# Performance work log

Measured on AMD Instinct MI355X. Metric: run time of the kernel, lower is better.

Reference implementation:

```python
import jax, jax.numpy as jnp
import numpy as np

V, D, B, L = 100000, 64, 4096, 200

def setup_inputs() -> dict:
    key = jax.random.key(0)
    ks = jax.random.split(key, 10)
    s = 0.05  # keep activations in a sane range for sigmoid
    return {
        "item_ids": jax.random.randint(ks[0], (B,), 0, V),
        "history": jax.random.randint(ks[1], (B, L), 0, V),
        "hist_len": jax.random.randint(ks[2], (B,), 1, L + 1),
        "emb_table": jax.random.normal(ks[3], (V, D), jnp.float32) * s,
        "aW1": jax.random.normal(ks[4], (3 * D, D), jnp.float32) * s,
        "ab1": jnp.zeros((D,), jnp.float32),
        "aW2": jax.random.normal(ks[5], (D, 1), jnp.float32) * s,
        "ab2": jnp.zeros((1,), jnp.float32),
        "fW1": jax.random.normal(ks[6], (3 * D, 128), jnp.float32) * s,
        "fb1": jnp.zeros((128,), jnp.float32),
        "fW2": jax.random.normal(ks[7], (128, 64), jnp.float32) * s,
        "fb2": jnp.zeros((64,), jnp.float32),
        "fW3": jax.random.normal(ks[8], (64, 1), jnp.float32) * s,
        "fb3": jnp.zeros((1,), jnp.float32),
    }

def reference(item_ids, history, hist_len, emb_table, aW1, ab1, aW2, ab2,
              fW1, fb1, fW2, fb2, fW3, fb3):
    target = emb_table[item_ids]                      # [B, D]
    hist = emb_table[history]                         # [B, L, D]
    # original pads short histories with zero rows -> zero the padded tail
    mask = (jnp.arange(hist.shape[1])[None, :] < hist_len[:, None]).astype(hist.dtype)
    hist = hist * mask[..., None]
    tgt = jnp.broadcast_to(target[:, None, :], hist.shape)     # [B, L, D]
    # attention_fc takes 3*D features: (hist, target, hist*target)
    feat = jnp.concatenate([hist, tgt, hist * tgt], axis=-1)   # [B, L, 3D]
    h = jax.nn.relu(feat @ aW1 + ab1)                 # [B, L, D]
    scores = (h @ aW2 + ab2)[..., 0]                  # [B, L]
    # faithful to original: softmax over full padded length (no length mask)
    w = jax.nn.softmax(scores, axis=1)
    pooled = jnp.einsum('bl,bld->bd', w, hist)        # [B, D]
    comb = jnp.concatenate([target, pooled, pooled - target], axis=-1)  # [B, 3D]
    z = jax.nn.relu(comb @ fW1 + fb1)
    z = jax.nn.relu(z @ fW2 + fb2)
    return jax.nn.sigmoid(z @ fW3 + fb3)              # [B, 1]
```

## Files before the change

kernel.cpp:

```cpp
#include <hip/hip_runtime.h>
#include <hip/hip_bf16.h>

#define NV 100000
#define ND 64
#define NB 4096
#define NL 200
#define MT 13

typedef __bf16 bf16_t;
typedef __bf16 bf16x8 __attribute__((ext_vector_type(8)));
typedef __bf16 bf16x4 __attribute__((ext_vector_type(4)));
typedef float f32x4 __attribute__((ext_vector_type(4)));

#define TB_ELEMS ((long)NV * ND)
#define TBV (TB_ELEMS / 8)
#define FT1 (128 * 192)
#define FT2 (64 * 128)
#define ZPV 64
#define CVT_TASKS (TBV + FT1 + FT2 + ZPV)

__global__ __launch_bounds__(256)
void cvt_kernel(const float* __restrict__ emb,
                const float* __restrict__ fW1,
                const float* __restrict__ fW2,
                bf16_t* __restrict__ tb,
                bf16_t* __restrict__ fW1T,
                bf16_t* __restrict__ fW2T,
                bf16_t* __restrict__ zpage)
{
    long t = (long)blockIdx.x * 256 + threadIdx.x;
    if (t >= CVT_TASKS) return;
    if (t < TBV) {
        long i = t * 8;
        f32x4 a0 = *(const f32x4*)(emb + i);
        f32x4 a1 = *(const f32x4*)(emb + i + 4);
        bf16x8 o;
#pragma unroll
        for (int j = 0; j < 4; ++j) { o[j] = (bf16_t)a0[j]; o[j + 4] = (bf16_t)a1[j]; }
        *(bf16x8*)(tb + i) = o;
    } else {
        int u = (int)(t - TBV);
        if (u < FT1) {
            int n = u / 192, k = u - n * 192;
            fW1T[u] = (bf16_t)fW1[k * 128 + n];
        } else if (u < FT1 + FT2) {
            int u2 = u - FT1;
            int n = u2 >> 7, k = u2 & 127;
            fW2T[u2] = (bf16_t)fW2[k * 64 + n];
        } else {
            int u3 = u - FT1 - FT2;
            *(bf16x8*)(zpage + u3 * 8) = (bf16x8)(bf16_t)0.f;
        }
    }
}

__global__ __launch_bounds__(512, 4)
void din_kernel1(const int* __restrict__ item_ids,
                 const int* __restrict__ history,
                 const int* __restrict__ hist_len,
                 const float* __restrict__ emb,
                 const bf16_t* __restrict__ tb,
                 const bf16_t* __restrict__ zpage,
                 const float* __restrict__ aW1,
                 const float* __restrict__ ab1,
                 const float* __restrict__ aW2,
                 const bf16_t* __restrict__ fW1T, const float* __restrict__ fb1,
                 const bf16_t* __restrict__ fW2T, const float* __restrict__ fb2,
                 const float* __restrict__ fW3, const float* __restrict__ fb3,
                 float* __restrict__ out)
{
    __shared__ __align__(16) bf16_t histA[2][208 * 64];
    __shared__ __align__(16) bf16_t wbT[2][64 * 64];
    __shared__ float tgt[2][64];
    __shared__ __align__(16) float scores[2][208];
    __shared__ float wts[2][208];
    __shared__ float pp2[2][256];
    __shared__ float red[2][8];
    __shared__ float cb2[2][64];

    bf16_t* comb16 = (bf16_t*)wbT;
    bf16_t* z1s    = (bf16_t*)wbT + 3200;
    float*  z2f    = (float*)((bf16_t*)wbT + 5376);

    const int b0  = blockIdx.x * 2;
    const int tid = threadIdx.x;
    const int len0 = hist_len[b0];
    const int len1 = hist_len[b0 + 1];

    const int wave = tid >> 6, lane = tid & 63;
    const int col  = lane & 15, quad = lane >> 4;

    if (tid < 128) {
        int bx = tid >> 6, d = tid & 63;
        tgt[bx][d] = emb[(long)item_ids[b0 + bx] * ND + d];
    }

    {
        const int r = lane >> 3;
        const int c = lane & 7;
#pragma unroll
        for (int j = 0; j < 7; ++j) {
            const int R = wave * 52 + j * 8;
            const int nrows = (j == 6) ? 4 : 8;
            const int l  = R + r;
            const int bx = (l >= 208);
            const int lr = l - (bx ? 208 : 0);
            const int lenx = bx ? len1 : len0;
            const bf16_t* gsrc;
            if (lr < lenx) {
                int idx = history[(long)(b0 + bx) * NL + lr];
                gsrc = tb + (long)idx * ND + ((c ^ (lr & 7)) * 8);
            } else {
                gsrc = zpage + c * 8;
            }
            if (r < nrows) {
                __builtin_amdgcn_global_load_lds(
                    (const __attribute__((address_space(1))) void*)gsrc,
                    (__attribute__((address_space(3))) void*)(&histA[0][0] + (long)R * 64),
                    16, 0, 0);
            }
        }
    }

    {
        const int bx = wave & 1;
        const int n  = ((wave >> 1) << 4) | col;
        const int kq = quad;
        const long t0 = (long)item_ids[b0 + bx] * ND;
        f32x4 tka = *(const f32x4*)(emb + t0 + kq * 16);
        f32x4 tkb = *(const f32x4*)(emb + t0 + kq * 16 + 4);
        f32x4 tkc = *(const f32x4*)(emb + t0 + kq * 16 + 8);
        f32x4 tkd = *(const f32x4*)(emb + t0 + kq * 16 + 12);
        float csum = 0.f;
        bf16x8 w0v, w1v;
#pragma unroll
        for (int i = 0; i < 16; ++i) {
            int k = kq * 16 + i;
            float tk = (i < 4) ? tka[i] : (i < 8) ? tkb[i - 4]
                     : (i < 12) ? tkc[i - 8] : tkd[i - 12];
            float ah = aW1[k * 64 + n];
            float am = aW1[(64 + k) * 64 + n];
            float ap = aW1[(128 + k) * 64 + n];
            float wv = ah + tk * ap;
            if (i < 8) w0v[i] = (bf16_t)wv; else w1v[i - 8] = (bf16_t)wv;
            csum += tk * am;
        }
        const int S = (n & 7) << 3;
        *(bf16x8*)&wbT[bx][n * 64 + ((kq * 16    ) ^ S)] = w0v;
        *(bf16x8*)&wbT[bx][n * 64 + ((kq * 16 + 8) ^ S)] = w1v;
        csum += __shfl_xor(csum, 16, 64);
        csum += __shfl_xor(csum, 32, 64);
        if (kq == 0) cb2[bx][n] = ab1[n] + csum;
    }
    __syncthreads();

    {
        const int bx = wave & 1;
        bf16x8 afrag[4][2];
#pragma unroll
        for (int nt = 0; nt < 4; ++nt) {
            const int n = nt * 16 + col;
            const int S = (n & 7) << 3;
#pragma unroll
            for (int kb = 0; kb < 2; ++kb)
                afrag[nt][kb] = *(const bf16x8*)&wbT[bx][n * 64 + ((kb * 32 + quad * 8) ^ S)];
        }
        float cv[4][4], a2[4][4];
#pragma unroll
        for (int nt = 0; nt < 4; ++nt)
#pragma unroll
            for (int i = 0; i < 4; ++i) {
                const int no = nt * 16 + quad * 4 + i;
                cv[nt][i] = cb2[bx][no];
                a2[nt][i] = aW2[no];
            }

        for (int mt = (wave >> 1); mt < MT; mt += 4) {
            const int l = mt * 16 + col;
            const int S = (l & 7) << 3;
            const bf16_t* base = &histA[bx][l * 64];
            bf16x8 bf0 = *(const bf16x8*)&base[(     quad * 8) ^ S];
            bf16x8 bf1 = *(const bf16x8*)&base[(32 + quad * 8) ^ S];
            float sc = 0.f;
#pragma unroll
            for (int nt = 0; nt < 4; ++nt) {
                f32x4 acc = {cv[nt][0], cv[nt][1], cv[nt][2], cv[nt][3]};
                acc = __builtin_amdgcn_mfma_f32_16x16x32_bf16(afrag[nt][0], bf0, acc, 0, 0, 0);
                acc = __builtin_amdgcn_mfma_f32_16x16x32_bf16(afrag[nt][1], bf1, acc, 0, 0, 0);
#pragma unroll
                for (int i = 0; i < 4; ++i) {
                    float h = acc[i] > 0.f ? acc[i] : 0.f;
                    sc += h * a2[nt][i];
                }
            }
            sc += __shfl_xor(sc, 16, 64);
            sc += __shfl_xor(sc, 32, 64);
            if (quad == 0) scores[bx][mt * 16 + col] = sc;
        }
    }
    __syncthreads();

    {
        const int bx = tid >> 8, t = tid & 255;
        float s = (t < NL) ? scores[bx][t] : -1e30f;
        float m = s;
        for (int off = 32; off > 0; off >>= 1) m = fmaxf(m, __shfl_xor(m, off, 64));
        float e = (t < NL) ? __expf(s - m) : 0.f;
        if (t < NL) wts[bx][t] = e;
        else if (t < 208) wts[bx][t] = 0.f;
        float ss = e;
        for (int off = 32; off > 0; off >>= 1) ss += __shfl_xor(ss, off, 64);
        if ((t & 63) == 0) { red[bx][t >> 6] = m; red[bx][4 + (t >> 6)] = ss; }
    }
    __syncthreads();

    bf16x8 bw1[6]; float b1v;
    bf16x8 bw2[4]; float b2v = 0.f;
    {
        const int n = wave * 16 + col;
#pragma unroll
        for (int ks = 0; ks < 6; ++ks)
            bw1[ks] = *(const bf16x8*)&fW1T[(long)n * 192 + ks * 32 + quad * 8];
        b1v = fb1[n];
        if (wave < 4) {
            const int n2 = wave * 16 + col;
#pragma unroll
            for (int ks = 0; ks < 4; ++ks)
                bw2[ks] = *(const bf16x8*)&fW2T[(long)n2 * 128 + ks * 32 + quad * 8];
            b2v = fb2[n2];
        }
    }

    {
        const int bx = tid >> 8, t = tid & 255;
        const int c = t & 15;
        const int g = t >> 4;
        const int w4 = (tid >> 6) & 3;
        const float m0 = red[bx][0], m1 = red[bx][1], m2 = red[bx][2], m3 = red[bx][3];
        const float mg = fmaxf(fmaxf(m0, m1), fmaxf(m2, m3));
        float sc0 = __expf(m0 - mg), sc1 = __expf(m1 - mg);
        float sc2 = __expf(m2 - mg), sc3 = __expf(m3 - mg);
        const float rtot = 1.f / (sc0 * red[bx][4] + sc1 * red[bx][5] +
                                  sc2 * red[bx][6] + sc3 * red[bx][7]);
        sc0 *= rtot; sc1 *= rtot; sc2 *= rtot; sc3 *= rtot;
        f32x4 acc = {0.f, 0.f, 0.f, 0.f};
#pragma unroll
        for (int j = 0; j < 13; ++j) {
            const int l = g + j * 16;
            const float scj = (j < 4) ? sc0 : (j < 8) ? sc1 : (j < 12) ? sc2 : sc3;
            const float wl = wts[bx][l] * scj;
            bf16x4 v = *(const bf16x4*)&histA[bx][l * 64 + ((c * 4) ^ ((l & 7) << 3))];
#pragma unroll
            for (int k = 0; k < 4; ++k) acc[k] += wl * (float)v[k];
        }
#pragma unroll
        for (int k = 0; k < 4; ++k) {
            acc[k] += __shfl_xor(acc[k], 16, 64);
            acc[k] += __shfl_xor(acc[k], 32, 64);
        }
        if ((tid & 63) < 16) *(f32x4*)&pp2[bx][w4 * 64 + c * 4] = acc;
    }
    __syncthreads();

    {
        const int bx = tid >> 8, t = tid & 255;
        if (t < 192) {
            const int d = t & 63;
            float v;
            if (t < 64) v = tgt[bx][d];
            else {
                float pl = pp2[bx][d] + pp2[bx][64 + d] + pp2[bx][128 + d] + pp2[bx][192 + d];
                v = (t < 128) ? pl : pl - tgt[bx][d];
            }
            comb16[bx * 200 + t] = (bf16_t)v;
        }
    }
    __syncthreads();

    {
        f32x4 acc = {b1v, b1v, b1v, b1v};
#pragma unroll
        for (int ks = 0; ks < 6; ++ks) {
            bf16x8 a = *(const bf16x8*)&comb16[col * 200 + ks * 32 + quad * 8];
            acc = __builtin_amdgcn_mfma_f32_16x16x32_bf16(a, bw1[ks], acc, 0, 0, 0);
        }
        const int n = wave * 16 + col;
#pragma unroll
        for (int i = 0; i < 4; ++i) {
            const int m = quad * 4 + i;
            if (m < 2) z1s[m * 136 + n] = (bf16_t)fmaxf(acc[i], 0.f);
        }
    }
    __syncthreads();

    {
        if (wave < 4) {
            f32x4 acc = {b2v, b2v, b2v, b2v};
#pragma unroll
            for (int ks = 0; ks < 4; ++ks) {
                bf16x8 a = *(const bf16x8*)&z1s[col * 136 + ks * 32 + quad * 8];
                acc = __builtin_amdgcn_mfma_f32_16x16x32_bf16(a, bw2[ks], acc, 0, 0, 0);
            }
            const int n2 = wave * 16 + col;
#pragma unroll
            for (int i = 0; i < 4; ++i) {
                const int m = quad * 4 + i;
                if (m < 2) z2f[m * 64 + n2] = fmaxf(acc[i], 0.f);
            }
        }
    }
    __syncthreads();

    if (tid < 128) {
        const int bx = tid >> 6, j = tid & 63;
        float s = z2f[bx * 64 + j] * fW3[j];
        for (int off = 32; off > 0; off >>= 1) s += __shfl_xor(s, off, 64);
        if (j == 0) out[b0 + bx] = 1.f / (1.f + __expf(-(s + fb3[0])));
    }
}

extern "C" void kernel_launch(void* const* d_in, const int* in_sizes, int n_in,
                              void* d_out, int out_size, void* d_ws, size_t ws_size,
                              hipStream_t stream) {
    const int*   item_ids = (const int*)d_in[0];
    const int*   history  = (const int*)d_in[1];
    const int*   hist_len = (const int*)d_in[2];
    const float* emb      = (const float*)d_in[3];
    const float* aW1      = (const float*)d_in[4];
    const float* ab1      = (const float*)d_in[5];
    const float* aW2      = (const float*)d_in[6];
    const float* fW1      = (const float*)d_in[8];
    const float* fb1      = (const float*)d_in[9];
    const float* fW2      = (const float*)d_in[10];
    const float* fb2      = (const float*)d_in[11];
    const float* fW3      = (const float*)d_in[12];
    const float* fb3      = (const float*)d_in[13];

    bf16_t* tb    = (bf16_t*)d_ws;
    bf16_t* fW1T  = tb + TB_ELEMS;
    bf16_t* fW2T  = fW1T + FT1;
    bf16_t* zpage = fW2T + FT2;

    cvt_kernel<<<(int)((CVT_TASKS + 255) / 256), 256, 0, stream>>>(
        emb, fW1, fW2, tb, fW1T, fW2T, zpage);
    din_kernel1<<<NB / 2, 512, 0, stream>>>(item_ids, history, hist_len, emb, tb,
                                            zpage, aW1, ab1, aW2,
                                            fW1T, fb1, fW2T, fb2, fW3, fb3,
                                            (float*)d_out);
}
```

Before: 145.1 us.

## Skip padded history rows and replace async LDS gather with register staging

Replaces the global_load_lds gather (which pulled zero-page rows for padding) with per-thread register loads that fetch only valid history rows, issued before the weight-prep phase and stored to LDS after it. The attention MLP loop now runs only over 16-row tiles covering the actual history length. Padded positions get one constant score computed once from the bias term, and the pooling loop breaks early past the length. This reduces MFMA work and gather traffic for short histories, at the cost of higher register pressure from holding eight 16-byte vectors per thread across the weight-prep code.

```diff
diff --git a/kernel.cpp b/kernel.cpp
--- a/kernel.cpp
+++ b/kernel.cpp
@@ -16,8 +16,7 @@
 #define TBV (TB_ELEMS / 8)
 #define FT1 (128 * 192)
 #define FT2 (64 * 128)
-#define ZPV 64
-#define CVT_TASKS (TBV + FT1 + FT2 + ZPV)
+#define CVT_TASKS (TBV + FT1 + FT2)
 
 __global__ __launch_bounds__(256)
 void cvt_kernel(const float* __restrict__ emb,
@@ -25,8 +24,7 @@
                 const float* __restrict__ fW2,
                 bf16_t* __restrict__ tb,
                 bf16_t* __restrict__ fW1T,
-                bf16_t* __restrict__ fW2T,
-                bf16_t* __restrict__ zpage)
+                bf16_t* __restrict__ fW2T)
 {
     long t = (long)blockIdx.x * 256 + threadIdx.x;
     if (t >= CVT_TASKS) return;
@@ -43,13 +41,10 @@
         if (u < FT1) {
             int n = u / 192, k = u - n * 192;
             fW1T[u] = (bf16_t)fW1[k * 128 + n];
-        } else if (u < FT1 + FT2) {
+        } else {
             int u2 = u - FT1;
             int n = u2 >> 7, k = u2 & 127;
             fW2T[u2] = (bf16_t)fW2[k * 64 + n];
-        } else {
-            int u3 = u - FT1 - FT2;
-            *(bf16x8*)(zpage + u3 * 8) = (bf16x8)(bf16_t)0.f;
         }
     }
 }
@@ -60,7 +55,6 @@
                  const int* __restrict__ hist_len,
                  const float* __restrict__ emb,
                  const bf16_t* __restrict__ tb,
-                 const bf16_t* __restrict__ zpage,
                  const float* __restrict__ aW1,
                  const float* __restrict__ ab1,
                  const float* __restrict__ aW2,
@@ -77,6 +71,7 @@
     __shared__ float pp2[2][256];
     __shared__ float red[2][8];
     __shared__ float cb2[2][64];
+    __shared__ float spadS[2];
 
     bf16_t* comb16 = (bf16_t*)wbT;
     bf16_t* z1s    = (bf16_t*)wbT + 3200;
@@ -90,37 +85,29 @@
     const int wave = tid >> 6, lane = tid & 63;
     const int col  = lane & 15, quad = lane >> 4;
 
-    if (tid < 128) {
-        int bx = tid >> 6, d = tid & 63;
-        tgt[bx][d] = emb[(long)item_ids[b0 + bx] * ND + d];
-    }
-
-    {
-        const int r = lane >> 3;
-        const int c = lane & 7;
-#pragma unroll
-        for (int j = 0; j < 7; ++j) {
-            const int R = wave * 52 + j * 8;
-            const int nrows = (j == 6) ? 4 : 8;
-            const int l  = R + r;
-            const int bx = (l >= 208);
-            const int lr = l - (bx ? 208 : 0);
-            const int lenx = bx ? len1 : len0;
-            const bf16_t* gsrc;
-            if (lr < lenx) {
-                int idx = history[(long)(b0 + bx) * NL + lr];
-                gsrc = tb + (long)idx * ND + ((c ^ (lr & 7)) * 8);
-            } else {
-                gsrc = zpage + c * 8;
-            }
-            if (r < nrows) {
-                __builtin_amdgcn_global_load_lds(
-                    (const __attribute__((address_space(1))) void*)gsrc,
-                    (__attribute__((address_space(3))) void*)(&histA[0][0] + (long)R * 64),
-                    16, 0, 0);
-            }
-        }
-    }
+    const int p  = tid & 1;
+    const int s  = tid >> 1;
+    const int bxA  = (s >= 208);
+    const int lA   = s - bxA * 208;
+    const int lB   = s + 48;
+    const int lenA = bxA ? len1 : len0;
+    const bool vB  = (s < 160);
+    const bf16x8 z8 = (bf16x8)(bf16_t)0.f;
+    bf16x8 a0 = z8, a1 = z8, a2v = z8, a3 = z8;
+    bf16x8 c0 = z8, c1 = z8, c2 = z8, c3 = z8;
+    float tg = 0.f;
+    if (tid < 128) tg = emb[(long)item_ids[b0 + (tid >> 6)] * ND + (tid & 63)];
+    if (lA < lenA) {
+        const bf16_t* src = tb + (long)history[(long)(b0 + bxA) * NL + lA] * ND + p * 32;
+        a0  = *(const bf16x8*)(src);      a1 = *(const bf16x8*)(src + 8);
+        a2v = *(const bf16x8*)(src + 16); a3 = *(const bf16x8*)(src + 24);
+    }
+    if (vB && lB < len1) {
+        const bf16_t* src = tb + (long)history[(long)(b0 + 1) * NL + lB] * ND + p * 32;
+        c0 = *(const bf16x8*)(src);      c1 = *(const bf16x8*)(src + 8);
+        c2 = *(const bf16x8*)(src + 16); c3 = *(const bf16x8*)(src + 24);
+    }
+    __builtin_amdgcn_sched_barrier(0);
 
     {
         const int bx = wave & 1;
@@ -152,10 +139,34 @@
         csum += __shfl_xor(csum, 32, 64);
         if (kq == 0) cb2[bx][n] = ab1[n] + csum;
     }
-    __syncthreads();
-
-    {
-        const int bx = wave & 1;
+    __builtin_amdgcn_sched_barrier(0);
+
+    {
+        {
+            bf16_t* d = &histA[bxA][lA * 64];
+            const int S = (lA & 7) << 3;
+            *(bf16x8*)&d[(p * 32 +  0) ^ S] = a0;
+            *(bf16x8*)&d[(p * 32 +  8) ^ S] = a1;
+            *(bf16x8*)&d[(p * 32 + 16) ^ S] = a2v;
+            *(bf16x8*)&d[(p * 32 + 24) ^ S] = a3;
+        }
+        if (vB) {
+            bf16_t* d = &histA[1][lB * 64];
+            const int S = (lB & 7) << 3;
+            *(bf16x8*)&d[(p * 32 +  0) ^ S] = c0;
+            *(bf16x8*)&d[(p * 32 +  8) ^ S] = c1;
+            *(bf16x8*)&d[(p * 32 + 16) ^ S] = c2;
+            *(bf16x8*)&d[(p * 32 + 24) ^ S] = c3;
+        }
+        if (tid < 128) tgt[tid >> 6][tid & 63] = tg;
+    }
+    __syncthreads();
+
+    {
+        const int bx   = wave & 1;
+        const int lenx = bx ? len1 : len0;
+        const int T    = (lenx + 15) >> 4;
+
         bf16x8 afrag[4][2];
 #pragma unroll
         for (int nt = 0; nt < 4; ++nt) {
@@ -175,7 +186,17 @@
                 a2[nt][i] = aW2[no];
             }
 
-        for (int mt = (wave >> 1); mt < MT; mt += 4) {
+        float ps = 0.f;
+#pragma unroll
+        for (int nt = 0; nt < 4; ++nt)
+#pragma unroll
+            for (int i = 0; i < 4; ++i)
+                ps += fmaxf(cv[nt][i], 0.f) * a2[nt][i];
+        ps += __shfl_xor(ps, 16, 64);
+        ps += __shfl_xor(ps, 32, 64);
+        if (wave < 2 && lane == 0) spadS[bx] = ps;
+
+        for (int mt = (wave >> 1); mt < T; mt += 4) {
             const int l = mt * 16 + col;
             const int S = (l & 7) << 3;
             const bf16_t* base = &histA[bx][l * 64];
@@ -202,7 +223,9 @@
 
     {
         const int bx = tid >> 8, t = tid & 255;
-        float s = (t < NL) ? scores[bx][t] : -1e30f;
+        const int lx = bx ? len1 : len0;
+        const int TT = ((lx + 15) >> 4) << 4;
+        float s = (t < NL) ? ((t < TT) ? scores[bx][t] : spadS[bx]) : -1e30f;
         float m = s;
         for (int off = 32; off > 0; off >>= 1) m = fmaxf(m, __shfl_xor(m, off, 64));
         float e = (t < NL) ? __expf(s - m) : 0.f;
@@ -233,6 +256,7 @@
 
     {
         const int bx = tid >> 8, t = tid & 255;
+        const int lx = bx ? len1 : len0;
         const int c = t & 15;
         const int g = t >> 4;
         const int w4 = (tid >> 6) & 3;
@@ -246,6 +270,7 @@
         f32x4 acc = {0.f, 0.f, 0.f, 0.f};
 #pragma unroll
         for (int j = 0; j < 13; ++j) {
+            if ((j << 4) >= lx) break;
             const int l = g + j * 16;
             const float scj = (j < 4) ? sc0 : (j < 8) ? sc1 : (j < 12) ? sc2 : sc3;
             const float wl = wts[bx][l] * scj;
@@ -293,29 +318,27 @@
     }
     __syncthreads();
 
-    {
-        if (wave < 4) {
-            f32x4 acc = {b2v, b2v, b2v, b2v};
-#pragma unroll
-            for (int ks = 0; ks < 4; ++ks) {
-                bf16x8 a = *(const bf16x8*)&z1s[col * 136 + ks * 32 + quad * 8];
-                acc = __builtin_amdgcn_mfma_f32_16x16x32_bf16(a, bw2[ks], acc, 0, 0, 0);
-            }
-            const int n2 = wave * 16 + col;
-#pragma unroll
-            for (int i = 0; i < 4; ++i) {
-                const int m = quad * 4 + i;
-                if (m < 2) z2f[m * 64 + n2] = fmaxf(acc[i], 0.f);
-            }
+    if (wave < 4) {
+        f32x4 acc = {b2v, b2v, b2v, b2v};
+#pragma unroll
+        for (int ks = 0; ks < 4; ++ks) {
+            bf16x8 a = *(const bf16x8*)&z1s[col * 136 + ks * 32 + quad * 8];
+            acc = __builtin_amdgcn_mfma_f32_16x16x32_bf16(a, bw2[ks], acc, 0, 0, 0);
+        }
+        const int n2 = wave * 16 + col;
+#pragma unroll
+        for (int i = 0; i < 4; ++i) {
+            const int m = quad * 4 + i;
+            if (m < 2) z2f[m * 64 + n2] = fmaxf(acc[i], 0.f);
         }
     }
     __syncthreads();
 
     if (tid < 128) {
         const int bx = tid >> 6, j = tid & 63;
-        float s = z2f[bx * 64 + j] * fW3[j];
-        for (int off = 32; off > 0; off >>= 1) s += __shfl_xor(s, off, 64);
-        if (j == 0) out[b0 + bx] = 1.f / (1.f + __expf(-(s + fb3[0])));
+        float sv = z2f[bx * 64 + j] * fW3[j];
+        for (int off = 32; off > 0; off >>= 1) sv += __shfl_xor(sv, off, 64);
+        if (j == 0) out[b0 + bx] = 1.f / (1.f + __expf(-(sv + fb3[0])));
     }
 }
 
@@ -336,15 +359,14 @@
     const float* fW3      = (const float*)d_in[12];
     const float* fb3      = (const float*)d_in[13];
 
-    bf16_t* tb    = (bf16_t*)d_ws;
-    bf16_t* fW1T  = tb + TB_ELEMS;
-    bf16_t* fW2T  = fW1T + FT1;
-    bf16_t* zpage = fW2T + FT2;
-
-    cvt_kernel<<<(int)((CVT_TASKS + 255) / 256), 256, 0, stream>>>(
-        emb, fW1, fW2, tb, fW1T, fW2T, zpage);
+    bf16_t* tb   = (bf16_t*)d_ws;
+    bf16_t* fW1T = tb + TB_ELEMS;
+    bf16_t* fW2T = fW1T + FT1;
+
+    cvt_kernel<<<(int)((CVT_TASKS + 255) / 256), 256, 0, stream>>>(emb, fW1, fW2,
+                                                                   tb, fW1T, fW2T);
     din_kernel1<<<NB / 2, 512, 0, stream>>>(item_ids, history, hist_len, emb, tb,
-                                            zpage, aW1, ab1, aW2,
+                                            aW1, ab1, aW2,
                                             fW1T, fb1, fW2T, fb2, fW3, fb3,
                                             (float*)d_out);
 }
```

Result: faster. 142.0 us (-2.1%).
